# Kernel optimization log

Hardware: AMD Instinct MI355X
Metric: run time of the kernel (lower is better)

The kernel has to match this reference:

```python
import jax, jax.numpy as jnp
import numpy as np

N, E, D = 50000, 640000, 128
EPS = 1e-5


def setup_inputs() -> dict:
    key = jax.random.key(0)
    ks = jax.random.split(key, 16)
    s = 1.0 / np.sqrt(D)
    inp = {
        "x": jax.random.normal(ks[0], (N, D), dtype=jnp.float32),
        "edge_index": jax.random.randint(ks[1], (2, E), 0, N, dtype=jnp.int64),
        "edge_attr": jax.random.normal(ks[2], (E, D), dtype=jnp.float32),
        "Wu": jax.random.uniform(ks[3], (D, D), jnp.float32, -s, s),
        "bu": jnp.zeros((D,), jnp.float32),
        "Wv": jax.random.uniform(ks[4], (D, D), jnp.float32, -s, s),
        "bv": jnp.zeros((D,), jnp.float32),
        "WA": jax.random.uniform(ks[5], (D, D), jnp.float32, -s, s),
        "bA": jnp.zeros((D,), jnp.float32),
        "WB": jax.random.uniform(ks[6], (D, D), jnp.float32, -s, s),
        "bB": jnp.zeros((D,), jnp.float32),
        "WC": jax.random.uniform(ks[7], (D, D), jnp.float32, -s, s),
        "bC": jnp.zeros((D,), jnp.float32),
        "gn_gamma": jnp.ones((D,), jnp.float32),
        "gn_beta": jnp.zeros((D,), jnp.float32),
        "ge_gamma": jnp.ones((D,), jnp.float32),
        "ge_beta": jnp.zeros((D,), jnp.float32),
    }
    return inp


def _bn(h, gamma, beta):
    # training-mode BatchNorm1d over the node/edge (batch) axis, biased var
    mu = jnp.mean(h, axis=0)
    var = jnp.var(h, axis=0)
    return gamma * (h - mu) * jax.lax.rsqrt(var + EPS) + beta


def reference(x, edge_index, edge_attr, Wu, bu, Wv, bv, WA, bA, WB, bB, WC, bC,
              gn_gamma, gn_beta, ge_gamma, ge_beta):
    row, col = edge_index[0], edge_index[1]
    # edge update: A(e) + B(x[row]) + C(x[col])
    Bx = x @ WB.T + bB  # [N, D] transform then gather (cheaper than gather-then-GEMM)
    Cx = x @ WC.T + bC
    edge_in = (edge_attr @ WA.T + bA) + Bx[row] + Cx[col]
    edge_tmp = jax.nn.relu(_bn(edge_in, ge_gamma, ge_beta))
    edge_out = edge_attr + edge_tmp
    # gated message passing
    sigma_edge = jax.nn.sigmoid(edge_out)
    node_neighbor = x @ Wv.T + bv
    msg = sigma_edge * node_neighbor[col]  # [E, D]
    agg_msg = jax.ops.segment_sum(msg, row, num_segments=x.shape[0])
    node_in = (x @ Wu.T + bu) + agg_msg
    node_tmp = jax.nn.relu(_bn(node_in, gn_gamma, gn_beta))
    x_out = x + node_tmp
    return (x_out, edge_out)
```

## Files before the change

kernel.cpp:

```cpp
#include <hip/hip_runtime.h>
#include <math.h>

#define NN 50000
#define NE 640000
#define DD 128

#define OFF_UVBC 0L
#define OFF_AGG   25600000L
#define OFF_WPACK 32000000L
#define OFF_BPACK 32065536L
#define OFF_STATS 32066048L

#define IO_PERM 0
#define IO_OFFS 640000
#define IO_CUR  692064
#define IO_CNT  744128

__global__ void k_prep(const float* __restrict__ Wu, const float* __restrict__ Wv,
                       const float* __restrict__ WB, const float* __restrict__ WC,
                       const float* __restrict__ bu, const float* __restrict__ bv,
                       const float* __restrict__ bB, const float* __restrict__ bC,
                       float* __restrict__ ws, int* __restrict__ cnt) {
  long i = (long)blockIdx.x * 256 + threadIdx.x;
  if (i < 65536) {
    int w = (int)(i >> 14), idx = (int)(i & 16383);
    const float* src = (w == 0) ? Wu : (w == 1) ? Wv : (w == 2) ? WB : WC;
    ws[OFF_WPACK + (long)w * 16384 + idx] = src[idx];
  } else if (i < 66048) {
    long j = i - 65536;
    int w = (int)(j >> 7), idx = (int)(j & 127);
    const float* src = (w == 0) ? bu : (w == 1) ? bv : (w == 2) ? bB : bC;
    ws[OFF_BPACK + j] = src[idx];
  } else if (i < 66560) {
    ws[OFF_STATS + (i - 66048)] = 0.f;
  } else if (i < 116560) {
    cnt[i - 66560] = 0;
  }
}

__global__ __launch_bounds__(256) void k_node_gemm(const float* __restrict__ x,
                                                   const float* __restrict__ Wp,
                                                   const float* __restrict__ bp,
                                                   float* __restrict__ out) {
  __shared__ float xt[32][132];
  __shared__ float wt[32][132];
  const int t = threadIdx.x;
  const int tx = t & 15, ty = t >> 4;
  const int rb = blockIdx.x * 128;
  const int fb = blockIdx.y * 128;
  float acc[8][8];
#pragma unroll
  for (int i = 0; i < 8; i++)
#pragma unroll
    for (int j = 0; j < 8; j++) acc[i][j] = 0.f;

  for (int kc = 0; kc < DD; kc += 32) {
#pragma unroll
    for (int s = 0; s < 4; s++) {
      int slot = t + s * 256;
      int r = slot >> 3;
      int kq = (slot & 7) << 2;
      int gr = rb + r;
      float4 v = make_float4(0.f, 0.f, 0.f, 0.f);
      if (gr < NN) v = *(const float4*)(x + (long)gr * DD + kc + kq);
      xt[kq][r] = v.x; xt[kq + 1][r] = v.y; xt[kq + 2][r] = v.z; xt[kq + 3][r] = v.w;
      float4 w = *(const float4*)(Wp + (long)(fb + r) * DD + kc + kq);
      wt[kq][r] = w.x; wt[kq + 1][r] = w.y; wt[kq + 2][r] = w.z; wt[kq + 3][r] = w.w;
    }
    __syncthreads();
#pragma unroll
    for (int k = 0; k < 32; k++) {
      float4 a0 = *(const float4*)&xt[k][ty * 8];
      float4 a1 = *(const float4*)&xt[k][ty * 8 + 4];
      float4 b0 = *(const float4*)&wt[k][tx * 8];
      float4 b1 = *(const float4*)&wt[k][tx * 8 + 4];
      float a[8] = {a0.x, a0.y, a0.z, a0.w, a1.x, a1.y, a1.z, a1.w};
      float b[8] = {b0.x, b0.y, b0.z, b0.w, b1.x, b1.y, b1.z, b1.w};
#pragma unroll
      for (int i = 0; i < 8; i++)
#pragma unroll
        for (int j = 0; j < 8; j++) acc[i][j] = fmaf(a[i], b[j], acc[i][j]);
    }
    __syncthreads();
  }
  float bb[8];
  *(float4*)&bb[0] = *(const float4*)(bp + fb + tx * 8);
  *(float4*)&bb[4] = *(const float4*)(bp + fb + tx * 8 + 4);
#pragma unroll
  for (int i = 0; i < 8; i++) {
    int gr = rb + ty * 8 + i;
    if (gr < NN) {
      float* op = out + (long)gr * 512 + fb + tx * 8;
      *(float4*)op = make_float4(acc[i][0] + bb[0], acc[i][1] + bb[1], acc[i][2] + bb[2], acc[i][3] + bb[3]);
      *(float4*)(op + 4) = make_float4(acc[i][4] + bb[4], acc[i][5] + bb[5], acc[i][6] + bb[6], acc[i][7] + bb[7]);
    }
  }
}

__global__ void k_hist(const int* __restrict__ rowi, int* __restrict__ cnt) {
  int e = blockIdx.x * 256 + threadIdx.x;
  if (e < NE) atomicAdd(&cnt[rowi[e]], 1);
}

__global__ __launch_bounds__(1024) void k_scan(const int* __restrict__ cnt,
                                               int* __restrict__ offs,
                                               int* __restrict__ cur) {
  __shared__ int wsum[17];
  const int t = threadIdx.x;
  const int lane = t & 63, w = t >> 6;
  int carry = 0;
  for (int base = 0; base < NN; base += 1024) {
    int idx = base + t;
    int v = (idx < NN) ? cnt[idx] : 0;
    int x = v;
#pragma unroll
    for (int off = 1; off < 64; off <<= 1) {
      int y = __shfl_up(x, off, 64);
      if (lane >= off) x += y;
    }
    if (lane == 63) wsum[w] = x;
    __syncthreads();
    if (t == 0) {
      int run = 0;
#pragma unroll
      for (int i = 0; i < 16; i++) { int tv = wsum[i]; wsum[i] = run; run += tv; }
      wsum[16] = run;
    }
    __syncthreads();
    int excl = x - v + wsum[w] + carry;
    if (idx < NN) { offs[idx] = excl; cur[idx] = excl; }
    carry += wsum[16];
    __syncthreads();
  }
  if (t == 0) offs[NN] = carry;
}

__global__ void k_scatter(const int* __restrict__ rowi, int* __restrict__ cur,
                          int* __restrict__ perm) {
  int e = blockIdx.x * 256 + threadIdx.x;
  if (e < NE) {
    int p = atomicAdd(&cur[rowi[e]], 1);
    perm[p] = e;
  }
}

__global__ __launch_bounds__(256) void k_edge_gemm(const float* __restrict__ ea,
                                                   const float* __restrict__ WA,
                                                   const float* __restrict__ bA,
                                                   const int* __restrict__ rowi,
                                                   const int* __restrict__ coli,
                                                   const float* __restrict__ UVBC,
                                                   float* __restrict__ edge_in,
                                                   float* __restrict__ esum,
                                                   float* __restrict__ esq) {
  __shared__ float xt[32][132];
  __shared__ float wt[32][132];
  const int t = threadIdx.x;
  const int tx = t & 15, ty = t >> 4;
  const int rb = blockIdx.x * 128;
  float acc[8][8];
#pragma unroll
  for (int i = 0; i < 8; i++)
#pragma unroll
    for (int j = 0; j < 8; j++) acc[i][j] = 0.f;

  for (int kc = 0; kc < DD; kc += 32) {
#pragma unroll
    for (int s = 0; s < 4; s++) {
      int slot = t + s * 256;
      int r = slot >> 3;
      int kq = (slot & 7) << 2;
      float4 v = *(const float4*)(ea + (long)(rb + r) * DD + kc + kq);
      xt[kq][r] = v.x; xt[kq + 1][r] = v.y; xt[kq + 2][r] = v.z; xt[kq + 3][r] = v.w;
      float4 w = *(const float4*)(WA + (long)r * DD + kc + kq);
      wt[kq][r] = w.x; wt[kq + 1][r] = w.y; wt[kq + 2][r] = w.z; wt[kq + 3][r] = w.w;
    }
    __syncthreads();
#pragma unroll
    for (int k = 0; k < 32; k++) {
      float4 a0 = *(const float4*)&xt[k][ty * 8];
      float4 a1 = *(const float4*)&xt[k][ty * 8 + 4];
      float4 b0 = *(const float4*)&wt[k][tx * 8];
      float4 b1 = *(const float4*)&wt[k][tx * 8 + 4];
      float a[8] = {a0.x, a0.y, a0.z, a0.w, a1.x, a1.y, a1.z, a1.w};
      float b[8] = {b0.x, b0.y, b0.z, b0.w, b1.x, b1.y, b1.z, b1.w};
#pragma unroll
      for (int i = 0; i < 8; i++)
#pragma unroll
        for (int j = 0; j < 8; j++) acc[i][j] = fmaf(a[i], b[j], acc[i][j]);
    }
    __syncthreads();
  }
  float bb[8];
  *(float4*)&bb[0] = *(const float4*)(bA + tx * 8);
  *(float4*)&bb[4] = *(const float4*)(bA + tx * 8 + 4);
  float s[8], q[8];
#pragma unroll
  for (int j = 0; j < 8; j++) { s[j] = 0.f; q[j] = 0.f; }
#pragma unroll
  for (int i = 0; i < 8; i++) {
    int e = rb + ty * 8 + i;
    int ri = rowi[e], ci = coli[e];
    const float* gB = UVBC + (long)ri * 512 + 256 + tx * 8;
    const float* gC = UVBC + (long)ci * 512 + 384 + tx * 8;
    float4 g0 = *(const float4*)gB, g1 = *(const float4*)(gB + 4);
    float4 h0 = *(const float4*)gC, h1 = *(const float4*)(gC + 4);
    float v[8];
    v[0] = acc[i][0] + bb[0] + g0.x + h0.x;
    v[1] = acc[i][1] + bb[1] + g0.y + h0.y;
    v[2] = acc[i][2] + bb[2] + g0.z + h0.z;
    v[3] = acc[i][3] + bb[3] + g0.w + h0.w;
    v[4] = acc[i][4] + bb[4] + g1.x + h1.x;
    v[5] = acc[i][5] + bb[5] + g1.y + h1.y;
    v[6] = acc[i][6] + bb[6] + g1.z + h1.z;
    v[7] = acc[i][7] + bb[7] + g1.w + h1.w;
    float* op = edge_in + (long)e * DD + tx * 8;
    *(float4*)op = make_float4(v[0], v[1], v[2], v[3]);
    *(float4*)(op + 4) = make_float4(v[4], v[5], v[6], v[7]);
#pragma unroll
    for (int j = 0; j < 8; j++) { s[j] += v[j]; q[j] += v[j] * v[j]; }
  }
#pragma unroll
  for (int j = 0; j < 8; j++) {
    s[j] += __shfl_xor(s[j], 16);
    s[j] += __shfl_xor(s[j], 32);
    q[j] += __shfl_xor(q[j], 16);
    q[j] += __shfl_xor(q[j], 32);
  }
  __syncthreads();
  float* red = &xt[0][0];
  if ((t & 63) < 16) {
    int w = t >> 6;
#pragma unroll
    for (int j = 0; j < 8; j++) {
      red[w * 128 + tx * 8 + j] = s[j];
      red[512 + w * 128 + tx * 8 + j] = q[j];
    }
  }
  __syncthreads();
  if (t < 128) {
    float ss = red[t] + red[128 + t] + red[256 + t] + red[384 + t];
    float qq = red[512 + t] + red[640 + t] + red[768 + t] + red[896 + t];
    atomicAdd(&esum[t], ss);
    atomicAdd(&esq[t], qq);
  }
}

__global__ void k_finalize(const float* __restrict__ sum, const float* __restrict__ sq,
                           const float* __restrict__ gamma, const float* __restrict__ beta,
                           float* __restrict__ scale, float* __restrict__ shift, float cnt) {
  int t = threadIdx.x;
  float mean = sum[t] / cnt;
  float var = sq[t] / cnt - mean * mean;
  float sc = gamma[t] * rsqrtf(var + 1e-5f);
  scale[t] = sc;
  shift[t] = beta[t] - mean * sc;
}

__global__ __launch_bounds__(256) void k_edge_final(const float* __restrict__ ea,
                                                    const float* __restrict__ escale,
                                                    const float* __restrict__ eshift,
                                                    float* __restrict__ eout) {
  const long TOT = (long)NE * DD / 4;
  const int f = (threadIdx.x & 31) * 4;
  float4 sc = *(const float4*)(escale + f);
  float4 sh = *(const float4*)(eshift + f);
  const long stride = (long)gridDim.x * 256;
  for (long i = (long)blockIdx.x * 256 + threadIdx.x; i < TOT; i += stride) {
    float4 ein = ((const float4*)eout)[i];
    float4 eav = ((const float4*)ea)[i];
    float4 eo;
    eo.x = eav.x + fmaxf(fmaf(ein.x, sc.x, sh.x), 0.f);
    eo.y = eav.y + fmaxf(fmaf(ein.y, sc.y, sh.y), 0.f);
    eo.z = eav.z + fmaxf(fmaf(ein.z, sc.z, sh.z), 0.f);
    eo.w = eav.w + fmaxf(fmaf(ein.w, sc.w, sh.w), 0.f);
    ((float4*)eout)[i] = eo;
  }
}

__global__ __launch_bounds__(256) void k_aggregate(const int* __restrict__ perm,
                                                   const int* __restrict__ offs,
                                                   const int* __restrict__ coli,
                                                   const float* __restrict__ eout,
                                                   const float* __restrict__ UVBC,
                                                   float* __restrict__ nodein,
                                                   float* __restrict__ nsum,
                                                   float* __restrict__ nsq) {
  __shared__ float red[2048];
  const int t = threadIdx.x;
  const int hw = t >> 5, lane = t & 31;
  const int f = lane * 4;
  float4 s = make_float4(0.f, 0.f, 0.f, 0.f);
  float4 q = make_float4(0.f, 0.f, 0.f, 0.f);
  for (int n = blockIdx.x * 8 + hw; n < NN; n += gridDim.x * 8) {
    int beg = offs[n], end = offs[n + 1];
    float4 acc = make_float4(0.f, 0.f, 0.f, 0.f);
    for (int i = beg; i < end; i++) {
      int e = perm[i];
      int ci = coli[e];
      float4 eo = *(const float4*)(eout + (long)e * DD + f);
      float4 vv = *(const float4*)(UVBC + (long)ci * 512 + 128 + f);
      float4 sg;
      sg.x = 1.f / (1.f + __expf(-eo.x));
      sg.y = 1.f / (1.f + __expf(-eo.y));
      sg.z = 1.f / (1.f + __expf(-eo.z));
      sg.w = 1.f / (1.f + __expf(-eo.w));
      acc.x = fmaf(sg.x, vv.x, acc.x);
      acc.y = fmaf(sg.y, vv.y, acc.y);
      acc.z = fmaf(sg.z, vv.z, acc.z);
      acc.w = fmaf(sg.w, vv.w, acc.w);
    }
    float4 u = *(const float4*)(UVBC + (long)n * 512 + f);
    float4 v = make_float4(acc.x + u.x, acc.y + u.y, acc.z + u.z, acc.w + u.w);
    *(float4*)(nodein + (long)n * DD + f) = v;
    s.x += v.x; s.y += v.y; s.z += v.z; s.w += v.w;
    q.x += v.x * v.x; q.y += v.y * v.y; q.z += v.z * v.z; q.w += v.w * v.w;
  }
  *(float4*)&red[hw * 128 + f] = s;
  *(float4*)&red[1024 + hw * 128 + f] = q;
  __syncthreads();
  if (t < 128) {
    float ss = 0.f, qq = 0.f;
#pragma unroll
    for (int w = 0; w < 8; w++) {
      ss += red[w * 128 + t];
      qq += red[1024 + w * 128 + t];
    }
    atomicAdd(&nsum[t], ss);
    atomicAdd(&nsq[t], qq);
  }
}

__global__ __launch_bounds__(256) void k_node_final(const float* __restrict__ x,
                                                    const float* __restrict__ nodein,
                                                    const float* __restrict__ nscale,
                                                    const float* __restrict__ nshift,
                                                    float* __restrict__ xout) {
  const long TOT = (long)NN * DD / 4;
  const int f = (threadIdx.x & 31) * 4;
  float4 sc = *(const float4*)(nscale + f);
  float4 sh = *(const float4*)(nshift + f);
  const long stride = (long)gridDim.x * 256;
  for (long i = (long)blockIdx.x * 256 + threadIdx.x; i < TOT; i += stride) {
    float4 xi = ((const float4*)x)[i];
    float4 v = ((const float4*)nodein)[i];
    float4 o;
    o.x = xi.x + fmaxf(fmaf(v.x, sc.x, sh.x), 0.f);
    o.y = xi.y + fmaxf(fmaf(v.y, sc.y, sh.y), 0.f);
    o.z = xi.z + fmaxf(fmaf(v.z, sc.z, sh.z), 0.f);
    o.w = xi.w + fmaxf(fmaf(v.w, sc.w, sh.w), 0.f);
    ((float4*)xout)[i] = o;
  }
}

extern "C" void kernel_launch(void* const* d_in, const int* in_sizes, int n_in,
                              void* d_out, int out_size, void* d_ws, size_t ws_size,
                              hipStream_t stream) {
  const float* x = (const float*)d_in[0];
  const int* ei = (const int*)d_in[1];
  const float* ea = (const float*)d_in[2];
  const float* Wu = (const float*)d_in[3];
  const float* bu = (const float*)d_in[4];
  const float* Wv = (const float*)d_in[5];
  const float* bv = (const float*)d_in[6];
  const float* WA = (const float*)d_in[7];
  const float* bA = (const float*)d_in[8];
  const float* WB = (const float*)d_in[9];
  const float* bB = (const float*)d_in[10];
  const float* WC = (const float*)d_in[11];
  const float* bC = (const float*)d_in[12];
  const float* gng = (const float*)d_in[13];
  const float* gnb = (const float*)d_in[14];
  const float* geg = (const float*)d_in[15];
  const float* geb = (const float*)d_in[16];
  const int* rowi = ei;
  const int* coli = ei + NE;

  float* ws = (float*)d_ws;
  float* out = (float*)d_out;
  float* eout = out + (long)NN * DD;
  float* UVBC = ws + OFF_UVBC;
  float* nodein = ws + OFF_AGG;
  float* Wp = ws + OFF_WPACK;
  float* bp = ws + OFF_BPACK;
  float* st = ws + OFF_STATS;
  float* esum = st, * esq = st + 128, * nsum = st + 256, * nsq = st + 384;
  float* escale = st + 512, * eshift = st + 640, * nscale = st + 768, * nshift = st + 896;

  int* iout = (int*)d_out;
  int* perm = iout + IO_PERM;
  int* offs = iout + IO_OFFS;
  int* cur = iout + IO_CUR;
  int* cnt = iout + IO_CNT;

  k_prep<<<456, 256, 0, stream>>>(Wu, Wv, WB, WC, bu, bv, bB, bC, ws, cnt);
  k_node_gemm<<<dim3(391, 4), 256, 0, stream>>>(x, Wp, bp, UVBC);
  k_hist<<<2500, 256, 0, stream>>>(rowi, cnt);
  k_scan<<<1, 1024, 0, stream>>>(cnt, offs, cur);
  k_scatter<<<2500, 256, 0, stream>>>(rowi, cur, perm);
  k_edge_gemm<<<5000, 256, 0, stream>>>(ea, WA, bA, rowi, coli, UVBC, eout, esum, esq);
  k_finalize<<<1, 128, 0, stream>>>(esum, esq, geg, geb, escale, eshift, (float)NE);
  k_edge_final<<<4096, 256, 0, stream>>>(ea, escale, eshift, eout);
  k_aggregate<<<1024, 256, 0, stream>>>(perm, offs, coli, eout, UVBC, nodein, nsum, nsq);
  k_finalize<<<1, 128, 0, stream>>>(nsum, nsq, gng, gnb, nscale, nshift, (float)NN);
  k_node_final<<<2048, 256, 0, stream>>>(x, nodein, nscale, nshift, out);
}
```

Before: 1.330 ms.

## Use split-bf16 MFMA GEMMs, parallel scan, and fuse edge finalize into aggregation

Both the node and edge GEMMs move from shared-memory FP32 FMA tiling to MFMA bf16 instructions. Each operand is split into high and low bf16 parts and combined with three MFMAs to stay close to FP32 accuracy, with weights pre-split in the prep kernel. The single-block node-count scan becomes a three-kernel multi-block scan. The edge BN/ReLU/residual pass is folded into the aggregation kernel, which removes a full read and write of the edge tensor. The risks are the changed precision of the split-bf16 products and edge-GEMM epilogue stores that are now strided per lane rather than float4-vectorised.

```diff
diff --git a/kernel.cpp b/kernel.cpp
--- a/kernel.cpp
+++ b/kernel.cpp
@@ -5,147 +5,134 @@
 #define NE 640000
 #define DD 128
 
-#define OFF_UVBC 0L
-#define OFF_AGG   25600000L
-#define OFF_WPACK 32000000L
-#define OFF_BPACK 32065536L
-#define OFF_STATS 32066048L
+#define OFF_UVBC   0L
+#define OFF_NODEIN 25600000L
+#define OFF_WNH    32000000L
+#define OFF_WNL    32032768L
+#define OFF_WAH    32065536L
+#define OFF_WAL    32073728L
+#define OFF_BN     32081920L
+#define OFF_STATS  32082432L
 
 #define IO_PERM 0
 #define IO_OFFS 640000
-#define IO_CUR  692064
-#define IO_CNT  744128
+#define IO_CUR  692000
+#define IO_CNT  744000
+#define IO_AUX  796000
+#define NBLK_SCAN 196
+
+typedef __attribute__((ext_vector_type(4))) float f32x4;
+typedef __attribute__((ext_vector_type(8))) short short8v;
+
+__device__ inline short f2bf(float x) {
+  unsigned u = __float_as_uint(x);
+  return (short)((u + 0x7fffu + ((u >> 16) & 1u)) >> 16);
+}
+__device__ inline float bf2f(short b) {
+  return __uint_as_float(((unsigned)(unsigned short)b) << 16);
+}
 
 __global__ void k_prep(const float* __restrict__ Wu, const float* __restrict__ Wv,
                        const float* __restrict__ WB, const float* __restrict__ WC,
+                       const float* __restrict__ WAw,
                        const float* __restrict__ bu, const float* __restrict__ bv,
                        const float* __restrict__ bB, const float* __restrict__ bC,
                        float* __restrict__ ws, int* __restrict__ cnt) {
   long i = (long)blockIdx.x * 256 + threadIdx.x;
+  short* WnH = (short*)(ws + OFF_WNH);
+  short* WnL = (short*)(ws + OFF_WNL);
+  short* WAH = (short*)(ws + OFF_WAH);
+  short* WAL = (short*)(ws + OFF_WAL);
   if (i < 65536) {
-    int w = (int)(i >> 14), idx = (int)(i & 16383);
-    const float* src = (w == 0) ? Wu : (w == 1) ? Wv : (w == 2) ? WB : WC;
-    ws[OFF_WPACK + (long)w * 16384 + idx] = src[idx];
-  } else if (i < 66048) {
+    int fidx = (int)(i >> 7), k = (int)(i & 127);
+    int wsel = fidx >> 7, frow = fidx & 127;
+    const float* src = (wsel == 0) ? Wu : (wsel == 1) ? Wv : (wsel == 2) ? WB : WC;
+    float v = src[frow * 128 + k];
+    short hb = f2bf(v);
+    WnH[i] = hb; WnL[i] = f2bf(v - bf2f(hb));
+  } else if (i < 81920) {
     long j = i - 65536;
-    int w = (int)(j >> 7), idx = (int)(j & 127);
-    const float* src = (w == 0) ? bu : (w == 1) ? bv : (w == 2) ? bB : bC;
-    ws[OFF_BPACK + j] = src[idx];
-  } else if (i < 66560) {
-    ws[OFF_STATS + (i - 66048)] = 0.f;
-  } else if (i < 116560) {
-    cnt[i - 66560] = 0;
+    float v = WAw[j];
+    short hb = f2bf(v);
+    WAH[j] = hb; WAL[j] = f2bf(v - bf2f(hb));
+  } else if (i < 82432) {
+    long j = i - 81920;
+    int wsel = (int)(j >> 7), k = (int)(j & 127);
+    const float* src = (wsel == 0) ? bu : (wsel == 1) ? bv : (wsel == 2) ? bB : bC;
+    ws[OFF_BN + j] = src[k];
+  } else if (i < 83456) {
+    ws[OFF_STATS + (i - 82432)] = 0.f;
+  } else if (i < 133456) {
+    cnt[i - 83456] = 0;
   }
 }
 
 __global__ __launch_bounds__(256) void k_node_gemm(const float* __restrict__ x,
-                                                   const float* __restrict__ Wp,
-                                                   const float* __restrict__ bp,
-                                                   float* __restrict__ out) {
-  __shared__ float xt[32][132];
-  __shared__ float wt[32][132];
-  const int t = threadIdx.x;
-  const int tx = t & 15, ty = t >> 4;
-  const int rb = blockIdx.x * 128;
-  const int fb = blockIdx.y * 128;
-  float acc[8][8];
-#pragma unroll
-  for (int i = 0; i < 8; i++)
-#pragma unroll
-    for (int j = 0; j < 8; j++) acc[i][j] = 0.f;
-
-  for (int kc = 0; kc < DD; kc += 32) {
-#pragma unroll
-    for (int s = 0; s < 4; s++) {
-      int slot = t + s * 256;
-      int r = slot >> 3;
-      int kq = (slot & 7) << 2;
-      int gr = rb + r;
-      float4 v = make_float4(0.f, 0.f, 0.f, 0.f);
-      if (gr < NN) v = *(const float4*)(x + (long)gr * DD + kc + kq);
-      xt[kq][r] = v.x; xt[kq + 1][r] = v.y; xt[kq + 2][r] = v.z; xt[kq + 3][r] = v.w;
-      float4 w = *(const float4*)(Wp + (long)(fb + r) * DD + kc + kq);
-      wt[kq][r] = w.x; wt[kq + 1][r] = w.y; wt[kq + 2][r] = w.z; wt[kq + 3][r] = w.w;
-    }
-    __syncthreads();
-#pragma unroll
-    for (int k = 0; k < 32; k++) {
-      float4 a0 = *(const float4*)&xt[k][ty * 8];
-      float4 a1 = *(const float4*)&xt[k][ty * 8 + 4];
-      float4 b0 = *(const float4*)&wt[k][tx * 8];
-      float4 b1 = *(const float4*)&wt[k][tx * 8 + 4];
-      float a[8] = {a0.x, a0.y, a0.z, a0.w, a1.x, a1.y, a1.z, a1.w};
-      float b[8] = {b0.x, b0.y, b0.z, b0.w, b1.x, b1.y, b1.z, b1.w};
-#pragma unroll
-      for (int i = 0; i < 8; i++)
-#pragma unroll
-        for (int j = 0; j < 8; j++) acc[i][j] = fmaf(a[i], b[j], acc[i][j]);
-    }
-    __syncthreads();
-  }
-  float bb[8];
-  *(float4*)&bb[0] = *(const float4*)(bp + fb + tx * 8);
-  *(float4*)&bb[4] = *(const float4*)(bp + fb + tx * 8 + 4);
-#pragma unroll
-  for (int i = 0; i < 8; i++) {
-    int gr = rb + ty * 8 + i;
-    if (gr < NN) {
-      float* op = out + (long)gr * 512 + fb + tx * 8;
-      *(float4*)op = make_float4(acc[i][0] + bb[0], acc[i][1] + bb[1], acc[i][2] + bb[2], acc[i][3] + bb[3]);
-      *(float4*)(op + 4) = make_float4(acc[i][4] + bb[4], acc[i][5] + bb[5], acc[i][6] + bb[6], acc[i][7] + bb[7]);
-    }
-  }
-}
-
-__global__ void k_hist(const int* __restrict__ rowi, int* __restrict__ cnt) {
-  int e = blockIdx.x * 256 + threadIdx.x;
-  if (e < NE) atomicAdd(&cnt[rowi[e]], 1);
-}
-
-__global__ __launch_bounds__(1024) void k_scan(const int* __restrict__ cnt,
-                                               int* __restrict__ offs,
-                                               int* __restrict__ cur) {
-  __shared__ int wsum[17];
-  const int t = threadIdx.x;
-  const int lane = t & 63, w = t >> 6;
-  int carry = 0;
-  for (int base = 0; base < NN; base += 1024) {
-    int idx = base + t;
-    int v = (idx < NN) ? cnt[idx] : 0;
-    int x = v;
-#pragma unroll
-    for (int off = 1; off < 64; off <<= 1) {
-      int y = __shfl_up(x, off, 64);
-      if (lane >= off) x += y;
-    }
-    if (lane == 63) wsum[w] = x;
-    __syncthreads();
-    if (t == 0) {
-      int run = 0;
-#pragma unroll
-      for (int i = 0; i < 16; i++) { int tv = wsum[i]; wsum[i] = run; run += tv; }
-      wsum[16] = run;
-    }
-    __syncthreads();
-    int excl = x - v + wsum[w] + carry;
-    if (idx < NN) { offs[idx] = excl; cur[idx] = excl; }
-    carry += wsum[16];
-    __syncthreads();
-  }
-  if (t == 0) offs[NN] = carry;
-}
-
-__global__ void k_scatter(const int* __restrict__ rowi, int* __restrict__ cur,
-                          int* __restrict__ perm) {
-  int e = blockIdx.x * 256 + threadIdx.x;
-  if (e < NE) {
-    int p = atomicAdd(&cur[rowi[e]], 1);
-    perm[p] = e;
+                                                   const short* __restrict__ WnH,
+                                                   const short* __restrict__ WnL,
+                                                   const float* __restrict__ bn,
+                                                   float* __restrict__ UVBC) {
+  const int t = threadIdx.x, w = t >> 6, lane = t & 63, cl = lane & 15, h = lane >> 4;
+  const long r0 = (long)blockIdx.x * 128 + w * 32;
+  short8v ahi[2][4], alo[2][4];
+#pragma unroll
+  for (int rb = 0; rb < 2; rb++) {
+    long row = r0 + rb * 16 + cl;
+    bool ok = row < NN;
+    const float* ap = x + row * 128 + h * 8;
+#pragma unroll
+    for (int ks = 0; ks < 4; ks++) {
+      f32x4 ra = ok ? *(const f32x4*)(ap + ks * 32) : (f32x4)0.f;
+      f32x4 rc = ok ? *(const f32x4*)(ap + ks * 32 + 4) : (f32x4)0.f;
+#pragma unroll
+      for (int j = 0; j < 4; j++) {
+        short hb = f2bf(ra[j]);
+        ahi[rb][ks][j] = hb; alo[rb][ks][j] = f2bf(ra[j] - bf2f(hb));
+        short hb2 = f2bf(rc[j]);
+        ahi[rb][ks][4 + j] = hb2; alo[rb][ks][4 + j] = f2bf(rc[j] - bf2f(hb2));
+      }
+    }
+  }
+#pragma unroll 1
+  for (int p = 0; p < 4; p++) {
+    f32x4 acc[2][8];
+#pragma unroll
+    for (int rb = 0; rb < 2; rb++)
+#pragma unroll
+      for (int cb = 0; cb < 8; cb++) acc[rb][cb] = (f32x4)0.f;
+#pragma unroll
+    for (int ks = 0; ks < 4; ks++) {
+#pragma unroll
+      for (int cb = 0; cb < 8; cb++) {
+        long boff = ((long)(p * 128 + cb * 16 + cl)) * 128 + ks * 32 + h * 8;
+        short8v bh = *(const short8v*)(WnH + boff);
+        short8v bl = *(const short8v*)(WnL + boff);
+#pragma unroll
+        for (int rb = 0; rb < 2; rb++) {
+          acc[rb][cb] = __builtin_amdgcn_mfma_f32_16x16x32_bf16(ahi[rb][ks], bh, acc[rb][cb], 0, 0, 0);
+          acc[rb][cb] = __builtin_amdgcn_mfma_f32_16x16x32_bf16(ahi[rb][ks], bl, acc[rb][cb], 0, 0, 0);
+          acc[rb][cb] = __builtin_amdgcn_mfma_f32_16x16x32_bf16(alo[rb][ks], bh, acc[rb][cb], 0, 0, 0);
+        }
+      }
+    }
+#pragma unroll
+    for (int cb = 0; cb < 8; cb++) {
+      int c = p * 128 + cb * 16 + cl;
+      float bias = bn[c];
+#pragma unroll
+      for (int rb = 0; rb < 2; rb++)
+#pragma unroll
+        for (int reg = 0; reg < 4; reg++) {
+          long row = r0 + rb * 16 + h * 4 + reg;
+          if (row < NN) UVBC[row * 512 + c] = acc[rb][cb][reg] + bias;
+        }
+    }
   }
 }
 
 __global__ __launch_bounds__(256) void k_edge_gemm(const float* __restrict__ ea,
-                                                   const float* __restrict__ WA,
+                                                   const short* __restrict__ WAH,
+                                                   const short* __restrict__ WAL,
                                                    const float* __restrict__ bA,
                                                    const int* __restrict__ rowi,
                                                    const int* __restrict__ coli,
@@ -153,96 +140,153 @@
                                                    float* __restrict__ edge_in,
                                                    float* __restrict__ esum,
                                                    float* __restrict__ esq) {
-  __shared__ float xt[32][132];
-  __shared__ float wt[32][132];
-  const int t = threadIdx.x;
-  const int tx = t & 15, ty = t >> 4;
-  const int rb = blockIdx.x * 128;
-  float acc[8][8];
-#pragma unroll
-  for (int i = 0; i < 8; i++)
-#pragma unroll
-    for (int j = 0; j < 8; j++) acc[i][j] = 0.f;
-
-  for (int kc = 0; kc < DD; kc += 32) {
-#pragma unroll
-    for (int s = 0; s < 4; s++) {
-      int slot = t + s * 256;
-      int r = slot >> 3;
-      int kq = (slot & 7) << 2;
-      float4 v = *(const float4*)(ea + (long)(rb + r) * DD + kc + kq);
-      xt[kq][r] = v.x; xt[kq + 1][r] = v.y; xt[kq + 2][r] = v.z; xt[kq + 3][r] = v.w;
-      float4 w = *(const float4*)(WA + (long)r * DD + kc + kq);
-      wt[kq][r] = w.x; wt[kq + 1][r] = w.y; wt[kq + 2][r] = w.z; wt[kq + 3][r] = w.w;
-    }
-    __syncthreads();
-#pragma unroll
-    for (int k = 0; k < 32; k++) {
-      float4 a0 = *(const float4*)&xt[k][ty * 8];
-      float4 a1 = *(const float4*)&xt[k][ty * 8 + 4];
-      float4 b0 = *(const float4*)&wt[k][tx * 8];
-      float4 b1 = *(const float4*)&wt[k][tx * 8 + 4];
-      float a[8] = {a0.x, a0.y, a0.z, a0.w, a1.x, a1.y, a1.z, a1.w};
-      float b[8] = {b0.x, b0.y, b0.z, b0.w, b1.x, b1.y, b1.z, b1.w};
-#pragma unroll
-      for (int i = 0; i < 8; i++)
-#pragma unroll
-        for (int j = 0; j < 8; j++) acc[i][j] = fmaf(a[i], b[j], acc[i][j]);
-    }
-    __syncthreads();
-  }
-  float bb[8];
-  *(float4*)&bb[0] = *(const float4*)(bA + tx * 8);
-  *(float4*)&bb[4] = *(const float4*)(bA + tx * 8 + 4);
+  __shared__ float red[2048];
+  const int t = threadIdx.x, w = t >> 6, lane = t & 63, cl = lane & 15, h = lane >> 4;
+  const long r0 = (long)blockIdx.x * 128 + w * 32;
+  short8v ahi[2][4], alo[2][4];
+#pragma unroll
+  for (int rb = 0; rb < 2; rb++) {
+    const float* ap = ea + (r0 + rb * 16 + cl) * 128 + h * 8;
+#pragma unroll
+    for (int ks = 0; ks < 4; ks++) {
+      f32x4 ra = *(const f32x4*)(ap + ks * 32);
+      f32x4 rc = *(const f32x4*)(ap + ks * 32 + 4);
+#pragma unroll
+      for (int j = 0; j < 4; j++) {
+        short hb = f2bf(ra[j]);
+        ahi[rb][ks][j] = hb; alo[rb][ks][j] = f2bf(ra[j] - bf2f(hb));
+        short hb2 = f2bf(rc[j]);
+        ahi[rb][ks][4 + j] = hb2; alo[rb][ks][4 + j] = f2bf(rc[j] - bf2f(hb2));
+      }
+    }
+  }
+  f32x4 acc[2][8];
+#pragma unroll
+  for (int rb = 0; rb < 2; rb++)
+#pragma unroll
+    for (int cb = 0; cb < 8; cb++) acc[rb][cb] = (f32x4)0.f;
+#pragma unroll
+  for (int ks = 0; ks < 4; ks++) {
+#pragma unroll
+    for (int cb = 0; cb < 8; cb++) {
+      long boff = ((long)(cb * 16 + cl)) * 128 + ks * 32 + h * 8;
+      short8v bh = *(const short8v*)(WAH + boff);
+      short8v bl = *(const short8v*)(WAL + boff);
+#pragma unroll
+      for (int rb = 0; rb < 2; rb++) {
+        acc[rb][cb] = __builtin_amdgcn_mfma_f32_16x16x32_bf16(ahi[rb][ks], bh, acc[rb][cb], 0, 0, 0);
+        acc[rb][cb] = __builtin_amdgcn_mfma_f32_16x16x32_bf16(ahi[rb][ks], bl, acc[rb][cb], 0, 0, 0);
+        acc[rb][cb] = __builtin_amdgcn_mfma_f32_16x16x32_bf16(alo[rb][ks], bh, acc[rb][cb], 0, 0, 0);
+      }
+    }
+  }
+  float ba[8];
+#pragma unroll
+  for (int cb = 0; cb < 8; cb++) ba[cb] = bA[cb * 16 + cl];
   float s[8], q[8];
 #pragma unroll
-  for (int j = 0; j < 8; j++) { s[j] = 0.f; q[j] = 0.f; }
-#pragma unroll
-  for (int i = 0; i < 8; i++) {
-    int e = rb + ty * 8 + i;
-    int ri = rowi[e], ci = coli[e];
-    const float* gB = UVBC + (long)ri * 512 + 256 + tx * 8;
-    const float* gC = UVBC + (long)ci * 512 + 384 + tx * 8;
-    float4 g0 = *(const float4*)gB, g1 = *(const float4*)(gB + 4);
-    float4 h0 = *(const float4*)gC, h1 = *(const float4*)(gC + 4);
-    float v[8];
-    v[0] = acc[i][0] + bb[0] + g0.x + h0.x;
-    v[1] = acc[i][1] + bb[1] + g0.y + h0.y;
-    v[2] = acc[i][2] + bb[2] + g0.z + h0.z;
-    v[3] = acc[i][3] + bb[3] + g0.w + h0.w;
-    v[4] = acc[i][4] + bb[4] + g1.x + h1.x;
-    v[5] = acc[i][5] + bb[5] + g1.y + h1.y;
-    v[6] = acc[i][6] + bb[6] + g1.z + h1.z;
-    v[7] = acc[i][7] + bb[7] + g1.w + h1.w;
-    float* op = edge_in + (long)e * DD + tx * 8;
-    *(float4*)op = make_float4(v[0], v[1], v[2], v[3]);
-    *(float4*)(op + 4) = make_float4(v[4], v[5], v[6], v[7]);
-#pragma unroll
-    for (int j = 0; j < 8; j++) { s[j] += v[j]; q[j] += v[j] * v[j]; }
-  }
-#pragma unroll
-  for (int j = 0; j < 8; j++) {
-    s[j] += __shfl_xor(s[j], 16);
-    s[j] += __shfl_xor(s[j], 32);
-    q[j] += __shfl_xor(q[j], 16);
-    q[j] += __shfl_xor(q[j], 32);
-  }
-  __syncthreads();
-  float* red = &xt[0][0];
+  for (int cb = 0; cb < 8; cb++) { s[cb] = 0.f; q[cb] = 0.f; }
+#pragma unroll
+  for (int rb = 0; rb < 2; rb++)
+#pragma unroll
+    for (int reg = 0; reg < 4; reg++) {
+      long e = r0 + rb * 16 + h * 4 + reg;
+      int ri = rowi[e], ci = coli[e];
+      const float* gB = UVBC + (long)ri * 512 + 256;
+      const float* gC = UVBC + (long)ci * 512 + 384;
+      float* op = edge_in + e * 128;
+#pragma unroll
+      for (int cb = 0; cb < 8; cb++) {
+        int c = cb * 16 + cl;
+        float v = acc[rb][cb][reg] + ba[cb] + gB[c] + gC[c];
+        op[c] = v;
+        s[cb] += v; q[cb] += v * v;
+      }
+    }
+#pragma unroll
+  for (int cb = 0; cb < 8; cb++) {
+    s[cb] += __shfl_xor(s[cb], 16); s[cb] += __shfl_xor(s[cb], 32);
+    q[cb] += __shfl_xor(q[cb], 16); q[cb] += __shfl_xor(q[cb], 32);
+  }
   if ((t & 63) < 16) {
-    int w = t >> 6;
-#pragma unroll
-    for (int j = 0; j < 8; j++) {
-      red[w * 128 + tx * 8 + j] = s[j];
-      red[512 + w * 128 + tx * 8 + j] = q[j];
+    int wv = t >> 6, c2 = t & 15;
+#pragma unroll
+    for (int cb = 0; cb < 8; cb++) {
+      red[wv * 128 + cb * 16 + c2] = s[cb];
+      red[1024 + wv * 128 + cb * 16 + c2] = q[cb];
     }
   }
   __syncthreads();
   if (t < 128) {
     float ss = red[t] + red[128 + t] + red[256 + t] + red[384 + t];
-    float qq = red[512 + t] + red[640 + t] + red[768 + t] + red[896 + t];
+    float qq = red[1024 + t] + red[1152 + t] + red[1280 + t] + red[1408 + t];
     atomicAdd(&esum[t], ss);
     atomicAdd(&esq[t], qq);
+  }
+}
+
+__global__ void k_hist(const int* __restrict__ rowi, int* __restrict__ cnt) {
+  int e = blockIdx.x * 256 + threadIdx.x;
+  if (e < NE) atomicAdd(&cnt[rowi[e]], 1);
+}
+
+__global__ __launch_bounds__(256) void k_scan1(const int* __restrict__ cnt,
+                                               int* __restrict__ offs,
+                                               int* __restrict__ aux) {
+  __shared__ int s[512];
+  const int t = threadIdx.x;
+  int idx = blockIdx.x * 256 + t;
+  int v = (idx < NN) ? cnt[idx] : 0;
+  int cur = 0, nxt = 256;
+  s[t] = v;
+  __syncthreads();
+  for (int off = 1; off < 256; off <<= 1) {
+    int val = s[cur + t];
+    if (t >= off) val += s[cur + t - off];
+    s[nxt + t] = val;
+    __syncthreads();
+    int tmp = cur; cur = nxt; nxt = tmp;
+  }
+  int incl = s[cur + t];
+  if (idx < NN) offs[idx] = incl - v;
+  if (t == 255) aux[blockIdx.x] = incl;
+}
+
+__global__ __launch_bounds__(256) void k_scan2(int* __restrict__ aux, int* __restrict__ offs) {
+  __shared__ int s[512];
+  const int t = threadIdx.x;
+  int v = (t < NBLK_SCAN) ? aux[t] : 0;
+  int cur = 0, nxt = 256;
+  s[t] = v;
+  __syncthreads();
+  for (int off = 1; off < 256; off <<= 1) {
+    int val = s[cur + t];
+    if (t >= off) val += s[cur + t - off];
+    s[nxt + t] = val;
+    __syncthreads();
+    int tmp = cur; cur = nxt; nxt = tmp;
+  }
+  int incl = s[cur + t];
+  if (t < NBLK_SCAN) aux[t] = incl - v;
+  if (t == 0) offs[NN] = NE;
+}
+
+__global__ void k_scan3(int* __restrict__ offs, const int* __restrict__ aux,
+                        int* __restrict__ cur) {
+  int idx = blockIdx.x * 256 + threadIdx.x;
+  if (idx < NN) {
+    int o = offs[idx] + aux[blockIdx.x];
+    offs[idx] = o;
+    cur[idx] = o;
+  }
+}
+
+__global__ void k_scatter(const int* __restrict__ rowi, int* __restrict__ cur,
+                          int* __restrict__ perm) {
+  int e = blockIdx.x * 256 + threadIdx.x;
+  if (e < NE) {
+    int p = atomicAdd(&cur[rowi[e]], 1);
+    perm[p] = e;
   }
 }
 
@@ -257,39 +301,21 @@
   shift[t] = beta[t] - mean * sc;
 }
 
-__global__ __launch_bounds__(256) void k_edge_final(const float* __restrict__ ea,
-                                                    const float* __restrict__ escale,
-                                                    const float* __restrict__ eshift,
-                                                    float* __restrict__ eout) {
-  const long TOT = (long)NE * DD / 4;
-  const int f = (threadIdx.x & 31) * 4;
+__global__ __launch_bounds__(256) void k_aggfinal(const int* __restrict__ perm,
+                                                  const int* __restrict__ offs,
+                                                  const int* __restrict__ coli,
+                                                  const float* __restrict__ ea,
+                                                  const float* __restrict__ escale,
+                                                  const float* __restrict__ eshift,
+                                                  const float* __restrict__ UVBC,
+                                                  float* __restrict__ eio,
+                                                  float* __restrict__ nodein,
+                                                  float* __restrict__ nsum,
+                                                  float* __restrict__ nsq) {
+  __shared__ float red[2048];
+  const int t = threadIdx.x, hw = t >> 5, lane = t & 31, f = lane * 4;
   float4 sc = *(const float4*)(escale + f);
   float4 sh = *(const float4*)(eshift + f);
-  const long stride = (long)gridDim.x * 256;
-  for (long i = (long)blockIdx.x * 256 + threadIdx.x; i < TOT; i += stride) {
-    float4 ein = ((const float4*)eout)[i];
-    float4 eav = ((const float4*)ea)[i];
-    float4 eo;
-    eo.x = eav.x + fmaxf(fmaf(ein.x, sc.x, sh.x), 0.f);
-    eo.y = eav.y + fmaxf(fmaf(ein.y, sc.y, sh.y), 0.f);
-    eo.z = eav.z + fmaxf(fmaf(ein.z, sc.z, sh.z), 0.f);
-    eo.w = eav.w + fmaxf(fmaf(ein.w, sc.w, sh.w), 0.f);
-    ((float4*)eout)[i] = eo;
-  }
-}
-
-__global__ __launch_bounds__(256) void k_aggregate(const int* __restrict__ perm,
-                                                   const int* __restrict__ offs,
-                                                   const int* __restrict__ coli,
-                                                   const float* __restrict__ eout,
-                                                   const float* __restrict__ UVBC,
-                                                   float* __restrict__ nodein,
-                                                   float* __restrict__ nsum,
-                                                   float* __restrict__ nsq) {
-  __shared__ float red[2048];
-  const int t = threadIdx.x;
-  const int hw = t >> 5, lane = t & 31;
-  const int f = lane * 4;
   float4 s = make_float4(0.f, 0.f, 0.f, 0.f);
   float4 q = make_float4(0.f, 0.f, 0.f, 0.f);
   for (int n = blockIdx.x * 8 + hw; n < NN; n += gridDim.x * 8) {
@@ -298,21 +324,23 @@
     for (int i = beg; i < end; i++) {
       int e = perm[i];
       int ci = coli[e];
-      float4 eo = *(const float4*)(eout + (long)e * DD + f);
+      float4 ein = *(const float4*)(eio + (long)e * 128 + f);
+      float4 eav = *(const float4*)(ea + (long)e * 128 + f);
+      float4 eo;
+      eo.x = eav.x + fmaxf(fmaf(ein.x, sc.x, sh.x), 0.f);
+      eo.y = eav.y + fmaxf(fmaf(ein.y, sc.y, sh.y), 0.f);
+      eo.z = eav.z + fmaxf(fmaf(ein.z, sc.z, sh.z), 0.f);
+      eo.w = eav.w + fmaxf(fmaf(ein.w, sc.w, sh.w), 0.f);
+      *(float4*)(eio + (long)e * 128 + f) = eo;
       float4 vv = *(const float4*)(UVBC + (long)ci * 512 + 128 + f);
-      float4 sg;
-      sg.x = 1.f / (1.f + __expf(-eo.x));
-      sg.y = 1.f / (1.f + __expf(-eo.y));
-      sg.z = 1.f / (1.f + __expf(-eo.z));
-      sg.w = 1.f / (1.f + __expf(-eo.w));
-      acc.x = fmaf(sg.x, vv.x, acc.x);
-      acc.y = fmaf(sg.y, vv.y, acc.y);
-      acc.z = fmaf(sg.z, vv.z, acc.z);
-      acc.w = fmaf(sg.w, vv.w, acc.w);
+      acc.x = fmaf(1.f / (1.f + __expf(-eo.x)), vv.x, acc.x);
+      acc.y = fmaf(1.f / (1.f + __expf(-eo.y)), vv.y, acc.y);
+      acc.z = fmaf(1.f / (1.f + __expf(-eo.z)), vv.z, acc.z);
+      acc.w = fmaf(1.f / (1.f + __expf(-eo.w)), vv.w, acc.w);
     }
     float4 u = *(const float4*)(UVBC + (long)n * 512 + f);
     float4 v = make_float4(acc.x + u.x, acc.y + u.y, acc.z + u.z, acc.w + u.w);
-    *(float4*)(nodein + (long)n * DD + f) = v;
+    *(float4*)(nodein + (long)n * 128 + f) = v;
     s.x += v.x; s.y += v.y; s.z += v.z; s.w += v.w;
     q.x += v.x * v.x; q.y += v.y * v.y; q.z += v.z * v.z; q.w += v.w * v.w;
   }
@@ -322,9 +350,9 @@
   if (t < 128) {
     float ss = 0.f, qq = 0.f;
 #pragma unroll
-    for (int w = 0; w < 8; w++) {
-      ss += red[w * 128 + t];
-      qq += red[1024 + w * 128 + t];
+    for (int wv = 0; wv < 8; wv++) {
+      ss += red[wv * 128 + t];
+      qq += red[1024 + wv * 128 + t];
     }
     atomicAdd(&nsum[t], ss);
     atomicAdd(&nsq[t], qq);
@@ -363,7 +391,7 @@
   const float* bu = (const float*)d_in[4];
   const float* Wv = (const float*)d_in[5];
   const float* bv = (const float*)d_in[6];
-  const float* WA = (const float*)d_in[7];
+  const float* WAw = (const float*)d_in[7];
   const float* bA = (const float*)d_in[8];
   const float* WB = (const float*)d_in[9];
   const float* bB = (const float*)d_in[10];
@@ -380,9 +408,12 @@
   float* out = (float*)d_out;
   float* eout = out + (long)NN * DD;
   float* UVBC = ws + OFF_UVBC;
-  float* nodein = ws + OFF_AGG;
-  float* Wp = ws + OFF_WPACK;
-  float* bp = ws + OFF_BPACK;
+  float* nodein = ws + OFF_NODEIN;
+  const short* WnH = (const short*)(ws + OFF_WNH);
+  const short* WnL = (const short*)(ws + OFF_WNL);
+  const short* WAH = (const short*)(ws + OFF_WAH);
+  const short* WAL = (const short*)(ws + OFF_WAL);
+  float* bn = ws + OFF_BN;
   float* st = ws + OFF_STATS;
   float* esum = st, * esq = st + 128, * nsum = st + 256, * nsq = st + 384;
   float* escale = st + 512, * eshift = st + 640, * nscale = st + 768, * nshift = st + 896;
@@ -392,16 +423,18 @@
   int* offs = iout + IO_OFFS;
   int* cur = iout + IO_CUR;
   int* cnt = iout + IO_CNT;
-
-  k_prep<<<456, 256, 0, stream>>>(Wu, Wv, WB, WC, bu, bv, bB, bC, ws, cnt);
-  k_node_gemm<<<dim3(391, 4), 256, 0, stream>>>(x, Wp, bp, UVBC);
+  int* aux = iout + IO_AUX;
+
+  k_prep<<<522, 256, 0, stream>>>(Wu, Wv, WB, WC, WAw, bu, bv, bB, bC, ws, cnt);
+  k_node_gemm<<<391, 256, 0, stream>>>(x, WnH, WnL, bn, UVBC);
   k_hist<<<2500, 256, 0, stream>>>(rowi, cnt);
-  k_scan<<<1, 1024, 0, stream>>>(cnt, offs, cur);
+  k_scan1<<<NBLK_SCAN, 256, 0, stream>>>(cnt, offs, aux);
+  k_scan2<<<1, 256, 0, stream>>>(aux, offs);
+  k_scan3<<<NBLK_SCAN, 256, 0, stream>>>(offs, aux, cur);
   k_scatter<<<2500, 256, 0, stream>>>(rowi, cur, perm);
-  k_edge_gemm<<<5000, 256, 0, stream>>>(ea, WA, bA, rowi, coli, UVBC, eout, esum, esq);
+  k_edge_gemm<<<5000, 256, 0, stream>>>(ea, WAH, WAL, bA, rowi, coli, UVBC, eout, esum, esq);
   k_finalize<<<1, 128, 0, stream>>>(esum, esq, geg, geb, escale, eshift, (float)NE);
-  k_edge_final<<<4096, 256, 0, stream>>>(ea, escale, eshift, eout);
-  k_aggregate<<<1024, 256, 0, stream>>>(perm, offs, coli, eout, UVBC, nodein, nsum, nsq);
+  k_aggfinal<<<1024, 256, 0, stream>>>(perm, offs, coli, ea, escale, eshift, UVBC, eout, nodein, nsum, nsq);
   k_finalize<<<1, 128, 0, stream>>>(nsum, nsq, gng, gnb, nscale, nshift, (float)NN);
   k_node_final<<<2048, 256, 0, stream>>>(x, nodein, nscale, nshift, out);
 }
```

After: 1.213 ms. -8.8%, faster.
